# Performance work log

Hardware: AMD Instinct MI355X
Metric: run time of the kernel (lower is better)

## Reference

```python
import jax, jax.numpy as jnp
import numpy as np

N = 8192        # num nodes
F_IN = 256      # input feature dim
HEADS = 4
HEAD_DIM = 64   # out_dim // heads = 256 // 4
NEG_SLOPE = 0.2 # standard GAT LeakyReLU slope


def setup_inputs() -> dict:
    key = jax.random.key(0)
    k1, k2, k3, k4, k5 = jax.random.split(key, 5)
    x = jax.random.normal(k1, (N, F_IN), dtype=jnp.float32)
    adj = jax.random.randint(k2, (N, N), 0, 2, dtype=jnp.int32)
    # glorot-uniform-ish scale for kernel
    lim = float(np.sqrt(6.0 / (F_IN + HEADS * HEAD_DIM)))
    W = jax.random.uniform(k3, (F_IN, HEADS, HEAD_DIM), dtype=jnp.float32, minval=-lim, maxval=lim)
    a_src = jax.random.normal(k4, (HEADS, HEAD_DIM), dtype=jnp.float32) * 0.1
    a_dst = jax.random.normal(k5, (HEADS, HEAD_DIM), dtype=jnp.float32) * 0.1
    bias = jnp.zeros((HEADS * HEAD_DIM,), dtype=jnp.float32)
    return {"x": x, "adj": adj, "W": W, "a_src": a_src, "a_dst": a_dst, "bias": bias}


def reference(x, adj, W, a_src, a_dst, bias):
    # per-head linear transform: [N, H, D]
    h = jnp.einsum('nf,fhd->nhd', x, W)
    # decomposed attention logits: e_ij = leaky_relu(a_src.h_i + a_dst.h_j)
    src = jnp.einsum('nhd,hd->nh', h, a_src)  # [N, H]
    dst = jnp.einsum('nhd,hd->nh', h, a_dst)  # [N, H]
    e = jax.nn.leaky_relu(src[:, None, :] + dst[None, :, :], NEG_SLOPE)  # [N, N, H]
    mask = adj[:, :, None] > 0
    e = jnp.where(mask, e, jnp.float32(-1e9))
    alpha = jax.nn.softmax(e, axis=1)  # softmax over neighbors j for each target i
    out = jnp.einsum('ijh,jhd->ihd', alpha, h)  # aggregate neighbor features
    return out.reshape(N, HEADS * HEAD_DIM) + bias  # concat heads + bias
```

## Files before the change

### kernel.cpp

```cpp
#include <hip/hip_runtime.h>
#include <cstdint>
#include <cstddef>

#define NN 8192
#define HEADS 4

typedef __attribute__((ext_vector_type(4))) float  f4;
typedef __attribute__((ext_vector_type(4))) int    i4;
typedef __attribute__((ext_vector_type(8))) short  short8;
typedef __attribute__((ext_vector_type(4))) unsigned short us4;
typedef __attribute__((ext_vector_type(4))) unsigned int   u4;
typedef unsigned int   uint32;
typedef unsigned short ushort16_t;

__device__ __forceinline__ unsigned short f2bf(float f) {
    unsigned int u = __builtin_bit_cast(unsigned int, f);
    u += 0x7FFFu + ((u >> 16) & 1u);
    return (unsigned short)(u >> 16);
}

__global__ void k0_convert(const float* __restrict__ x, const float* __restrict__ W,
                           unsigned short* __restrict__ xb, unsigned short* __restrict__ WT) {
    int b = blockIdx.x;
    if (b < 2048) {
        int idx = (b * 256 + threadIdx.x) * 4;
        f4 v = *(const f4*)(x + idx);
        us4 o;
        o.x = f2bf(v.x); o.y = f2bf(v.y); o.z = f2bf(v.z); o.w = f2bf(v.w);
        *(us4*)(xb + idx) = o;
    } else {
        int f = b - 2048;
        int c = threadIdx.x;
        WT[c * 256 + f] = f2bf(W[f * 256 + c]);
    }
}

__global__ __launch_bounds__(256) void kpack(const int* __restrict__ adj,
                                             uint32* __restrict__ adjP) {
    int gid = blockIdx.x * 256 + threadIdx.x;
    const int* p = adj + (size_t)gid * 32;
    uint32 w = 0;
    #pragma unroll
    for (int k = 0; k < 8; k++) {
        i4 v = *(const i4*)(p + k * 4);
        w |= (v.x != 0 ? 1u : 0u) << (k * 4 + 0);
        w |= (v.y != 0 ? 1u : 0u) << (k * 4 + 1);
        w |= (v.z != 0 ? 1u : 0u) << (k * 4 + 2);
        w |= (v.w != 0 ? 1u : 0u) << (k * 4 + 3);
    }
    adjP[gid] = w;
}

__global__ __launch_bounds__(256) void k1_hgemm(
    const unsigned short* __restrict__ xb, const unsigned short* __restrict__ WT,
    const float* __restrict__ aS, const float* __restrict__ aD,
    unsigned short* __restrict__ hF,
    float* __restrict__ sE, float* __restrict__ sE2,
    float* __restrict__ dE, float* __restrict__ dE2)
{
    const int tid  = threadIdx.x;
    const int head = tid >> 6;
    const int lane = tid & 63;
    const int col  = lane & 15;
    const int quad = lane >> 4;
    const int i0   = blockIdx.x * 32;

    const unsigned short* ar0 = xb + (size_t)(i0 + col) * 256 + quad * 8;
    const unsigned short* ar1 = ar0 + 16 * 256;
    const unsigned short* br  = WT + (size_t)(head * 64 + col) * 256 + quad * 8;

    f4 C[2][4];
    #pragma unroll
    for (int a = 0; a < 2; a++)
        #pragma unroll
        for (int b = 0; b < 4; b++) C[a][b] = f4{0.f, 0.f, 0.f, 0.f};

    #pragma unroll
    for (int kk = 0; kk < 256; kk += 32) {
        short8 a0 = *(const short8*)(ar0 + kk);
        short8 a1 = *(const short8*)(ar1 + kk);
        #pragma unroll
        for (int nt = 0; nt < 4; nt++) {
            short8 bf = *(const short8*)(br + nt * 16 * 256 + kk);
            C[0][nt] = __builtin_amdgcn_mfma_f32_16x16x32_bf16(a0, bf, C[0][nt], 0, 0, 0);
            C[1][nt] = __builtin_amdgcn_mfma_f32_16x16x32_bf16(a1, bf, C[1][nt], 0, 0, 0);
        }
    }

    float as_[4], ad_[4];
    #pragma unroll
    for (int nt = 0; nt < 4; nt++) {
        as_[nt] = aS[head * 64 + nt * 16 + col];
        ad_[nt] = aD[head * 64 + nt * 16 + col];
    }
    #pragma unroll
    for (int mt = 0; mt < 2; mt++) {
        #pragma unroll
        for (int r = 0; r < 4; r++) {
            float sv = 0.f, dv = 0.f;
            #pragma unroll
            for (int nt = 0; nt < 4; nt++) {
                sv += C[mt][nt][r] * as_[nt];
                dv += C[mt][nt][r] * ad_[nt];
            }
            #pragma unroll
            for (int m = 1; m < 16; m <<= 1) {
                sv += __shfl_xor(sv, m, 64);
                dv += __shfl_xor(dv, m, 64);
            }
            if (col == 0) {
                int i = i0 + mt * 16 + quad * 4 + r;
                float zs = sv * 1.4426950408889634f;
                float zd = dv * 1.4426950408889634f;
                sE [head * NN + i] = __builtin_amdgcn_exp2f(zs);
                sE2[head * NN + i] = __builtin_amdgcn_exp2f(0.2f * zs);
                dE [head * NN + i] = __builtin_amdgcn_exp2f(zd);
                dE2[head * NN + i] = __builtin_amdgcn_exp2f(0.2f * zd);
            }
        }
    }

    const size_t fbase = (((size_t)blockIdx.x * HEADS + head) * 4) * 512;
    #pragma unroll
    for (int mt = 0; mt < 2; mt++) {
        #pragma unroll
        for (int nt = 0; nt < 4; nt++) {
            #pragma unroll
            for (int r = 0; r < 4; r++) {
                int il = mt * 16 + quad * 4 + r;
                int qp = il >> 3;
                int t  = il & 7;
                hF[fbase + (size_t)nt * 512 + (qp * 16 + col) * 8 + t] =
                    f2bf(C[mt][nt][r]);
            }
        }
    }
}

__device__ __forceinline__ short8 build_w(uint32 bits,
                                          const f4& alo, const f4& ahi,
                                          const f4& blo, const f4& bhi,
                                          float es, float es2) {
    float aa[8] = {alo[0], alo[1], alo[2], alo[3], ahi[0], ahi[1], ahi[2], ahi[3]};
    float bb[8] = {blo[0], blo[1], blo[2], blo[3], bhi[0], bhi[1], bhi[2], bhi[3]};
    float e[8];
    #pragma unroll
    for (int t = 0; t < 8; t++) {
        float av = es  * aa[t];
        float bv = es2 * bb[t];
        float m  = fmaxf(av, bv);
        float mf = (float)((bits >> t) & 1u);
        e[t] = m * mf;
    }
    u4 pv;
    #pragma unroll
    for (int t = 0; t < 4; t++) {
        uint32 e0 = __builtin_bit_cast(uint32, e[2 * t])     + 0x8000u;
        uint32 e1 = __builtin_bit_cast(uint32, e[2 * t + 1]) + 0x8000u;
        pv[t] = __builtin_amdgcn_perm(e1, e0, 0x07060302u);
    }
    return __builtin_bit_cast(short8, pv);
}

__global__ __launch_bounds__(256, 4) void k2_gat(
    const uint32* __restrict__ adjP, const unsigned short* __restrict__ hF,
    const float* __restrict__ sE, const float* __restrict__ sE2,
    const float* __restrict__ dE, const float* __restrict__ dE2,
    float* __restrict__ Pout, float* __restrict__ PS, int jchunk)
{
    const int tid   = threadIdx.x;
    const int head  = tid >> 6;
    const int lane  = tid & 63;
    const int col   = lane & 15;
    const int quad  = lane >> 4;
    const int itile = blockIdx.x & 255;
    const int split = blockIdx.x >> 8;
    const int i0    = itile * 32;
    const int j0    = split * jchunk;

    const float es0  = sE [head * NN + i0 + col];
    const float es0b = sE2[head * NN + i0 + col];
    const float es1  = sE [head * NN + i0 + 16 + col];
    const float es1b = sE2[head * NN + i0 + 16 + col];

    const uint32* ap0 = adjP + (size_t)(i0 + col) * 256 + (j0 >> 5);
    const uint32* ap1 = ap0 + 16 * 256;
    const float* dEp  = dE  + head * NN + j0 + quad * 8;
    const float* dE2p = dE2 + head * NN + j0 + quad * 8;
    const unsigned short* hbase =
        hF + ((size_t)(j0 >> 5) * HEADS + head) * 4 * 512 + lane * 8;

    f4 acc[2][4];
    f4 accS[2];
    #pragma unroll
    for (int a = 0; a < 2; a++) {
        accS[a] = f4{0.f, 0.f, 0.f, 0.f};
        #pragma unroll
        for (int b = 0; b < 4; b++) acc[a][b] = f4{0.f, 0.f, 0.f, 0.f};
    }
    short8 ones;
    #pragma unroll
    for (int t = 0; t < 8; t++) ones[t] = (short)0x3F80;

    const int ngrp = jchunk >> 7;
    for (int g = 0; g < ngrp; ++g) {
        u4 aw0 = *(const u4*)(ap0 + g * 4);
        u4 aw1 = *(const u4*)(ap1 + g * 4);
        #pragma unroll
        for (int k = 0; k < 4; ++k) {
            const int jb = g * 4 + k;
            const float* dp  = dEp  + jb * 32;
            const float* dp2 = dE2p + jb * 32;
            f4 alo = *(const f4*)(dp);
            f4 ahi = *(const f4*)(dp + 4);
            f4 blo = *(const f4*)(dp2);
            f4 bhi = *(const f4*)(dp2 + 4);
            const unsigned short* hp = hbase + (size_t)jb * (HEADS * 4 * 512);
            short8 B0 = *(const short8*)(hp);
            short8 B1 = *(const short8*)(hp + 512);
            short8 B2 = *(const short8*)(hp + 1024);
            short8 B3 = *(const short8*)(hp + 1536);

            uint32 b0 = (aw0[k] >> (quad * 8)) & 0xFFu;
            uint32 b1 = (aw1[k] >> (quad * 8)) & 0xFFu;
            short8 af0 = build_w(b0, alo, ahi, blo, bhi, es0, es0b);
            short8 af1 = build_w(b1, alo, ahi, blo, bhi, es1, es1b);

            acc[0][0] = __builtin_amdgcn_mfma_f32_16x16x32_bf16(af0, B0, acc[0][0], 0, 0, 0);
            acc[0][1] = __builtin_amdgcn_mfma_f32_16x16x32_bf16(af0, B1, acc[0][1], 0, 0, 0);
            acc[0][2] = __builtin_amdgcn_mfma_f32_16x16x32_bf16(af0, B2, acc[0][2], 0, 0, 0);
            acc[0][3] = __builtin_amdgcn_mfma_f32_16x16x32_bf16(af0, B3, acc[0][3], 0, 0, 0);
            accS[0]   = __builtin_amdgcn_mfma_f32_16x16x32_bf16(af0, ones, accS[0], 0, 0, 0);
            acc[1][0] = __builtin_amdgcn_mfma_f32_16x16x32_bf16(af1, B0, acc[1][0], 0, 0, 0);
            acc[1][1] = __builtin_amdgcn_mfma_f32_16x16x32_bf16(af1, B1, acc[1][1], 0, 0, 0);
            acc[1][2] = __builtin_amdgcn_mfma_f32_16x16x32_bf16(af1, B2, acc[1][2], 0, 0, 0);
            acc[1][3] = __builtin_amdgcn_mfma_f32_16x16x32_bf16(af1, B3, acc[1][3], 0, 0, 0);
            accS[1]   = __builtin_amdgcn_mfma_f32_16x16x32_bf16(af1, ones, accS[1], 0, 0, 0);
        }
    }

    #pragma unroll
    for (int mt = 0; mt < 2; mt++) {
        #pragma unroll
        for (int nt = 0; nt < 4; nt++) {
            #pragma unroll
            for (int r = 0; r < 4; r++) {
                int row = i0 + mt * 16 + quad * 4 + r;
                Pout[((size_t)split * NN + row) * 256 + head * 64 + nt * 16 + col] =
                    acc[mt][nt][r];
            }
        }
        if (col == 0) {
            #pragma unroll
            for (int r = 0; r < 4; r++) {
                int row = i0 + mt * 16 + quad * 4 + r;
                PS[((size_t)split * NN + row) * HEADS + head] = accS[mt][r];
            }
        }
    }
}

__global__ void k3_norm(const float* __restrict__ Pout, const float* __restrict__ PS,
                        const float* __restrict__ bias, float* __restrict__ out,
                        int jsplit)
{
    int t  = blockIdx.x * 256 + threadIdx.x;
    int c4 = t * 4;
    int i    = c4 >> 8;
    int cb   = c4 & 255;
    int head = cb >> 6;
    f4 num = f4{0.f, 0.f, 0.f, 0.f};
    float den = 0.f;
    for (int s = 0; s < jsplit; s++) {
        num += *(const f4*)(Pout + ((size_t)s * NN + i) * 256 + cb);
        den += PS[((size_t)s * NN + i) * HEADS + head];
    }
    f4 bv = *(const f4*)(bias + cb);
    f4 o  = num * (1.0f / den) + bv;
    *(f4*)(out + c4) = o;
}

extern "C" void kernel_launch(void* const* d_in, const int* in_sizes, int n_in,
                              void* d_out, int out_size, void* d_ws, size_t ws_size,
                              hipStream_t stream) {
    (void)in_sizes; (void)n_in; (void)out_size;
    const float* x    = (const float*)d_in[0];
    const int*   adj  = (const int*)d_in[1];
    const float* W    = (const float*)d_in[2];
    const float* aS   = (const float*)d_in[3];
    const float* aD   = (const float*)d_in[4];
    const float* bias = (const float*)d_in[5];
    float* out = (float*)d_out;

    char* ws = (char*)d_ws;
    unsigned short* xb = (unsigned short*)(ws);
    unsigned short* WT = (unsigned short*)(ws +  4194304);
    unsigned short* hF = (unsigned short*)(ws +  4325376);
    float*  sE   = (float*)(ws +  8519680);
    float*  sE2  = (float*)(ws +  8650752);
    float*  dE   = (float*)(ws +  8781824);
    float*  dE2  = (float*)(ws +  8912896);
    uint32* adjP = (uint32*)(ws +  9043968);
    float*  PS   = (float*)(ws + 17432576);
    float*  Pout = (float*)(ws + 18481152);

    const size_t need8 = 18481152ull + 8ull * 8388608ull;
    const int jsplit = (ws_size >= need8) ? 8 : 4;
    const int jchunk = NN / jsplit;

    k0_convert<<<2304, 256, 0, stream>>>(x, W, xb, WT);
    kpack<<<8192, 256, 0, stream>>>(adj, adjP);
    k1_hgemm<<<256, 256, 0, stream>>>(xb, WT, aS, aD, hF, sE, sE2, dE, dE2);
    k2_gat<<<256 * jsplit, 256, 0, stream>>>(adjP, hF, sE, sE2, dE, dE2, Pout, PS, jchunk);
    k3_norm<<<2048, 256, 0, stream>>>(Pout, PS, bias, out, jsplit);
}
```

Baseline: 489.9 us.

## Pack adjacency as byte masks in MFMA fragment order for the GAT kernel

The adjacency packer now turns each int32 edge flag into a 0x00/0xFF byte mask and stages it through shared memory. It writes the masks in the exact per-lane MFMA fragment order, so the aggregation kernel loads 8 mask bytes per lane per 32-column block with one coalesced vector load. In build_w, the per-element bit extraction, int-to-float conversion and multiply are replaced by a byte-permute mask ANDed onto the packed bf16 weights, and the max/scale math is vectorised. The cost is an 8x larger adjacency buffer (64 MB instead of 8 MB bits), which adds memory traffic in both the packer and the GAT kernel. It also moves the workspace offsets, so the 8-way split now needs a larger workspace.

```diff
diff --git a/kernel.cpp b/kernel.cpp
--- a/kernel.cpp
+++ b/kernel.cpp
@@ -10,8 +10,8 @@
 typedef __attribute__((ext_vector_type(8))) short  short8;
 typedef __attribute__((ext_vector_type(4))) unsigned short us4;
 typedef __attribute__((ext_vector_type(4))) unsigned int   u4;
-typedef unsigned int   uint32;
-typedef unsigned short ushort16_t;
+typedef __attribute__((ext_vector_type(2))) unsigned int   u2;
+typedef unsigned int uint32;
 
 __device__ __forceinline__ unsigned short f2bf(float f) {
     unsigned int u = __builtin_bit_cast(unsigned int, f);
@@ -36,19 +36,40 @@
 }
 
 __global__ __launch_bounds__(256) void kpack(const int* __restrict__ adj,
-                                             uint32* __restrict__ adjP) {
-    int gid = blockIdx.x * 256 + threadIdx.x;
-    const int* p = adj + (size_t)gid * 32;
-    uint32 w = 0;
-    #pragma unroll
-    for (int k = 0; k < 8; k++) {
-        i4 v = *(const i4*)(p + k * 4);
-        w |= (v.x != 0 ? 1u : 0u) << (k * 4 + 0);
-        w |= (v.y != 0 ? 1u : 0u) << (k * 4 + 1);
-        w |= (v.z != 0 ? 1u : 0u) << (k * 4 + 2);
-        w |= (v.w != 0 ? 1u : 0u) << (k * 4 + 3);
-    }
-    adjP[gid] = w;
+                                             unsigned char* __restrict__ adjF) {
+    __shared__ uint32 tile[32 * 66];
+    const int itile = blockIdx.x >> 5;
+    const int jgrp  = blockIdx.x & 31;
+    const int i0 = itile * 32;
+    const int j0 = jgrp * 256;
+    const int tid = threadIdx.x;
+    const int rrow = tid >> 6;
+    const int jc   = (tid & 63) * 4;
+
+    #pragma unroll
+    for (int it = 0; it < 8; ++it) {
+        int row = it * 4 + rrow;
+        i4 v = *(const i4*)(adj + (size_t)(i0 + row) * NN + j0 + jc);
+        uint32 w = (v.x ? 0xFFu : 0u) | (v.y ? 0xFF00u : 0u) |
+                   (v.z ? 0xFF0000u : 0u) | (v.w ? 0xFF000000u : 0u);
+        tile[row * 66 + (jc >> 2)] = w;
+    }
+    __syncthreads();
+
+    const size_t bbase = (size_t)(itile * 256 + jgrp * 8) * 1024;
+    #pragma unroll
+    for (int k = 0; k < 4; ++k) {
+        int s    = k * 256 + tid;
+        int jbl  = s >> 7;
+        int r    = (s >> 6) & 1;
+        int lane = s & 63;
+        int col  = lane & 15, quad = lane >> 4;
+        int row  = r * 16 + col;
+        int c    = jbl * 8 + quad * 2;
+        uint32 w0 = tile[row * 66 + c];
+        uint32 w1 = tile[row * 66 + c + 1];
+        *(u2*)(adjF + bbase + (size_t)s * 8) = u2{w0, w1};
+    }
 }
 
 __global__ __launch_bounds__(256) void k1_hgemm(
@@ -137,33 +158,33 @@
     }
 }
 
-__device__ __forceinline__ short8 build_w(uint32 bits,
+__device__ __forceinline__ short8 build_w(const u2& ab,
                                           const f4& alo, const f4& ahi,
                                           const f4& blo, const f4& bhi,
                                           float es, float es2) {
-    float aa[8] = {alo[0], alo[1], alo[2], alo[3], ahi[0], ahi[1], ahi[2], ahi[3]};
-    float bb[8] = {blo[0], blo[1], blo[2], blo[3], bhi[0], bhi[1], bhi[2], bhi[3]};
-    float e[8];
-    #pragma unroll
-    for (int t = 0; t < 8; t++) {
-        float av = es  * aa[t];
-        float bv = es2 * bb[t];
-        float m  = fmaxf(av, bv);
-        float mf = (float)((bits >> t) & 1u);
-        e[t] = m * mf;
-    }
+    f4 esv  = f4{es, es, es, es};
+    f4 es2v = f4{es2, es2, es2, es2};
+    f4 x0 = esv * alo,  x1 = esv * ahi;
+    f4 y0 = es2v * blo, y1 = es2v * bhi;
+    f4 m0 = __builtin_elementwise_max(x0, y0);
+    f4 m1 = __builtin_elementwise_max(x1, y1);
+    float mm[8] = {m0[0], m0[1], m0[2], m0[3], m1[0], m1[1], m1[2], m1[3]};
     u4 pv;
     #pragma unroll
-    for (int t = 0; t < 4; t++) {
-        uint32 e0 = __builtin_bit_cast(uint32, e[2 * t])     + 0x8000u;
-        uint32 e1 = __builtin_bit_cast(uint32, e[2 * t + 1]) + 0x8000u;
-        pv[t] = __builtin_amdgcn_perm(e1, e0, 0x07060302u);
+    for (int k = 0; k < 4; ++k) {
+        uint32 src = (k < 2) ? ab.x : ab.y;
+        uint32 sel = (k & 1) ? 0x07070606u : 0x05050404u;
+        uint32 mkw = __builtin_amdgcn_perm(src, 0u, sel);
+        uint32 e0 = __builtin_bit_cast(uint32, mm[2 * k])     + 0x8000u;
+        uint32 e1 = __builtin_bit_cast(uint32, mm[2 * k + 1]) + 0x8000u;
+        uint32 packed = __builtin_amdgcn_perm(e1, e0, 0x07060302u);
+        pv[k] = packed & mkw;
     }
     return __builtin_bit_cast(short8, pv);
 }
 
 __global__ __launch_bounds__(256, 4) void k2_gat(
-    const uint32* __restrict__ adjP, const unsigned short* __restrict__ hF,
+    const unsigned char* __restrict__ adjF, const unsigned short* __restrict__ hF,
     const float* __restrict__ sE, const float* __restrict__ sE2,
     const float* __restrict__ dE, const float* __restrict__ dE2,
     float* __restrict__ Pout, float* __restrict__ PS, int jchunk)
@@ -183,8 +204,8 @@
     const float es1  = sE [head * NN + i0 + 16 + col];
     const float es1b = sE2[head * NN + i0 + 16 + col];
 
-    const uint32* ap0 = adjP + (size_t)(i0 + col) * 256 + (j0 >> 5);
-    const uint32* ap1 = ap0 + 16 * 256;
+    const unsigned char* abase =
+        adjF + (size_t)(itile * 256 + (j0 >> 5)) * 1024 + lane * 8;
     const float* dEp  = dE  + head * NN + j0 + quad * 8;
     const float* dE2p = dE2 + head * NN + j0 + quad * 8;
     const unsigned short* hbase =
@@ -202,41 +223,34 @@
     #pragma unroll
     for (int t = 0; t < 8; t++) ones[t] = (short)0x3F80;
 
-    const int ngrp = jchunk >> 7;
+    const int ngrp = jchunk >> 5;
+    #pragma unroll 2
     for (int g = 0; g < ngrp; ++g) {
-        u4 aw0 = *(const u4*)(ap0 + g * 4);
-        u4 aw1 = *(const u4*)(ap1 + g * 4);
-        #pragma unroll
-        for (int k = 0; k < 4; ++k) {
-            const int jb = g * 4 + k;
-            const float* dp  = dEp  + jb * 32;
-            const float* dp2 = dE2p + jb * 32;
-            f4 alo = *(const f4*)(dp);
-            f4 ahi = *(const f4*)(dp + 4);
-            f4 blo = *(const f4*)(dp2);
-            f4 bhi = *(const f4*)(dp2 + 4);
-            const unsigned short* hp = hbase + (size_t)jb * (HEADS * 4 * 512);
-            short8 B0 = *(const short8*)(hp);
-            short8 B1 = *(const short8*)(hp + 512);
-            short8 B2 = *(const short8*)(hp + 1024);
-            short8 B3 = *(const short8*)(hp + 1536);
-
-            uint32 b0 = (aw0[k] >> (quad * 8)) & 0xFFu;
-            uint32 b1 = (aw1[k] >> (quad * 8)) & 0xFFu;
-            short8 af0 = build_w(b0, alo, ahi, blo, bhi, es0, es0b);
-            short8 af1 = build_w(b1, alo, ahi, blo, bhi, es1, es1b);
-
-            acc[0][0] = __builtin_amdgcn_mfma_f32_16x16x32_bf16(af0, B0, acc[0][0], 0, 0, 0);
-            acc[0][1] = __builtin_amdgcn_mfma_f32_16x16x32_bf16(af0, B1, acc[0][1], 0, 0, 0);
-            acc[0][2] = __builtin_amdgcn_mfma_f32_16x16x32_bf16(af0, B2, acc[0][2], 0, 0, 0);
-            acc[0][3] = __builtin_amdgcn_mfma_f32_16x16x32_bf16(af0, B3, acc[0][3], 0, 0, 0);
-            accS[0]   = __builtin_amdgcn_mfma_f32_16x16x32_bf16(af0, ones, accS[0], 0, 0, 0);
-            acc[1][0] = __builtin_amdgcn_mfma_f32_16x16x32_bf16(af1, B0, acc[1][0], 0, 0, 0);
-            acc[1][1] = __builtin_amdgcn_mfma_f32_16x16x32_bf16(af1, B1, acc[1][1], 0, 0, 0);
-            acc[1][2] = __builtin_amdgcn_mfma_f32_16x16x32_bf16(af1, B2, acc[1][2], 0, 0, 0);
-            acc[1][3] = __builtin_amdgcn_mfma_f32_16x16x32_bf16(af1, B3, acc[1][3], 0, 0, 0);
-            accS[1]   = __builtin_amdgcn_mfma_f32_16x16x32_bf16(af1, ones, accS[1], 0, 0, 0);
-        }
+        u2 a0 = *(const u2*)(abase + (size_t)g * 1024);
+        u2 a1 = *(const u2*)(abase + (size_t)g * 1024 + 512);
+        f4 alo = *(const f4*)(dEp  + g * 32);
+        f4 ahi = *(const f4*)(dEp  + g * 32 + 4);
+        f4 blo = *(const f4*)(dE2p + g * 32);
+        f4 bhi = *(const f4*)(dE2p + g * 32 + 4);
+        const unsigned short* hp = hbase + (size_t)g * (HEADS * 4 * 512);
+        short8 B0 = *(const short8*)(hp);
+        short8 B1 = *(const short8*)(hp + 512);
+        short8 B2 = *(const short8*)(hp + 1024);
+        short8 B3 = *(const short8*)(hp + 1536);
+
+        short8 af0 = build_w(a0, alo, ahi, blo, bhi, es0, es0b);
+        short8 af1 = build_w(a1, alo, ahi, blo, bhi, es1, es1b);
+
+        acc[0][0] = __builtin_amdgcn_mfma_f32_16x16x32_bf16(af0, B0, acc[0][0], 0, 0, 0);
+        acc[0][1] = __builtin_amdgcn_mfma_f32_16x16x32_bf16(af0, B1, acc[0][1], 0, 0, 0);
+        acc[0][2] = __builtin_amdgcn_mfma_f32_16x16x32_bf16(af0, B2, acc[0][2], 0, 0, 0);
+        acc[0][3] = __builtin_amdgcn_mfma_f32_16x16x32_bf16(af0, B3, acc[0][3], 0, 0, 0);
+        accS[0]   = __builtin_amdgcn_mfma_f32_16x16x32_bf16(af0, ones, accS[0], 0, 0, 0);
+        acc[1][0] = __builtin_amdgcn_mfma_f32_16x16x32_bf16(af1, B0, acc[1][0], 0, 0, 0);
+        acc[1][1] = __builtin_amdgcn_mfma_f32_16x16x32_bf16(af1, B1, acc[1][1], 0, 0, 0);
+        acc[1][2] = __builtin_amdgcn_mfma_f32_16x16x32_bf16(af1, B2, acc[1][2], 0, 0, 0);
+        acc[1][3] = __builtin_amdgcn_mfma_f32_16x16x32_bf16(af1, B3, acc[1][3], 0, 0, 0);
+        accS[1]   = __builtin_amdgcn_mfma_f32_16x16x32_bf16(af1, ones, accS[1], 0, 0, 0);
     }
 
     #pragma unroll
@@ -300,17 +314,17 @@
     float*  sE2  = (float*)(ws +  8650752);
     float*  dE   = (float*)(ws +  8781824);
     float*  dE2  = (float*)(ws +  8912896);
-    uint32* adjP = (uint32*)(ws +  9043968);
-    float*  PS   = (float*)(ws + 17432576);
-    float*  Pout = (float*)(ws + 18481152);
-
-    const size_t need8 = 18481152ull + 8ull * 8388608ull;
+    unsigned char* adjF = (unsigned char*)(ws + 9043968);
+    float*  PS   = (float*)(ws + 76152832);
+    float*  Pout = (float*)(ws + 77201408);
+
+    const size_t need8 = 77201408ull + 8ull * 8388608ull;
     const int jsplit = (ws_size >= need8) ? 8 : 4;
     const int jchunk = NN / jsplit;
 
     k0_convert<<<2304, 256, 0, stream>>>(x, W, xb, WT);
-    kpack<<<8192, 256, 0, stream>>>(adj, adjP);
+    kpack<<<8192, 256, 0, stream>>>(adj, adjF);
     k1_hgemm<<<256, 256, 0, stream>>>(xb, WT, aS, aD, hF, sE, sE2, dE, dE2);
-    k2_gat<<<256 * jsplit, 256, 0, stream>>>(adjP, hF, sE, sE2, dE, dE2, Pout, PS, jchunk);
+    k2_gat<<<256 * jsplit, 256, 0, stream>>>(adjF, hF, sE, sE2, dE, dE2, Pout, PS, jchunk);
     k3_norm<<<2048, 256, 0, stream>>>(Pout, PS, bias, out, jsplit);
 }
```

Result: slower. 516.5 us (+5.4%).
